# Performance work log

Hardware: AMD Instinct MI355X
Metric: run time of the kernel (lower is better)

Reference implementation:

```python
import jax, jax.numpy as jnp
import numpy as np

N, E, G = 50000, 500000, 64
IN_F, H_F, HEADS, OUT_F = 128, 64, 4, 326000
NEG_SLOPE = 0.2


def _gat_layer(h, W, a_src, a_dst, b, src, dst):
    # h: [N, H_F]; W: [H_F, HEADS*H_F]; a_src/a_dst: [HEADS, H_F]; b: [H_F]
    x = (h @ W).reshape(N, HEADS, H_F)                      # per-head transform
    ls = jnp.einsum('nhc,hc->nh', x, a_src)                  # [N, HEADS]
    ld = jnp.einsum('nhc,hc->nh', x, a_dst)
    e = jax.nn.leaky_relu(ls[src] + ld[dst], NEG_SLOPE)      # [E', HEADS] edge logits
    m = jax.ops.segment_max(e, dst, num_segments=N)          # segment-softmax (stable)
    m = jnp.where(jnp.isfinite(m), m, 0.0)
    ex = jnp.exp(e - m[dst])
    denom = jax.ops.segment_sum(ex, dst, num_segments=N)
    alpha = ex / (denom[dst] + 1e-16)                        # [E', HEADS]
    out = jax.ops.segment_sum(x[src] * alpha[:, :, None], dst, num_segments=N)  # [N,HEADS,H_F]
    return out.mean(axis=1) + b                              # concat=False -> head mean + bias


def setup_inputs() -> dict:
    key = jax.random.key(0)
    ks = jax.random.split(key, 24)
    inp = {
        'x': jax.random.normal(ks[0], (N, IN_F), dtype=jnp.float32),
        'edge_index': jax.random.randint(ks[1], (2, E), 0, N, dtype=jnp.int32),
        'edge_attr': jax.random.normal(ks[2], (E, 16), dtype=jnp.float32),
        'batch': jnp.sort(jax.random.randint(ks[3], (N,), 0, G, dtype=jnp.int32)),
        'W_emb': jax.random.normal(ks[4], (IN_F, H_F), dtype=jnp.float32) * 0.05,
        'b_emb': jnp.zeros((H_F,), dtype=jnp.float32),
        'W_fc': jax.random.normal(ks[5], (H_F, OUT_F), dtype=jnp.float32) * 0.05,
        'b_fc': jnp.zeros((OUT_F,), dtype=jnp.float32),
    }
    for l in range(3):
        inp[f'W{l+1}'] = jax.random.normal(ks[6 + 4 * l], (H_F, HEADS * H_F), dtype=jnp.float32) * 0.05
        inp[f'a_src{l+1}'] = jax.random.normal(ks[7 + 4 * l], (HEADS, H_F), dtype=jnp.float32) * 0.1
        inp[f'a_dst{l+1}'] = jax.random.normal(ks[8 + 4 * l], (HEADS, H_F), dtype=jnp.float32) * 0.1
        inp[f'b{l+1}'] = jnp.zeros((H_F,), dtype=jnp.float32)
    return inp


def reference(x, edge_index, edge_attr, batch, W_emb, b_emb,
              W1, a_src1, a_dst1, b1, W2, a_src2, a_dst2, b2,
              W3, a_src3, a_dst3, b3, W_fc, b_fc):
    # add self loops (PyG GATConv default)
    loop = jnp.arange(N, dtype=edge_index.dtype)
    src = jnp.concatenate([edge_index[0], loop])
    dst = jnp.concatenate([edge_index[1], loop])

    h = x @ W_emb + b_emb
    for (W, a_s, a_d, b) in ((W1, a_src1, a_dst1, b1), (W2, a_src2, a_dst2, b2), (W3, a_src3, a_dst3, b3)):
        h = jax.nn.relu(_gat_layer(h, W, a_s, a_d, b, src, dst))

    # global mean pool over graphs
    sums = jax.ops.segment_sum(h, batch, num_segments=G)
    cnt = jax.ops.segment_sum(jnp.ones((N,), h.dtype), batch, num_segments=G)
    pooled = sums / jnp.maximum(cnt, 1.0)[:, None]
    # dropout is identity in eval mode
    return pooled @ W_fc + b_fc
```

## Files before the change

### kernel.cpp

```cpp
#include <hip/hip_runtime.h>

#define NN 50000
#define EE 500000
#define GG 64
#define IN_F 128
#define H_F 64
#define HEADS 4
#define OUT_F 326000
#define NEG 0.2f
#define SCAN_B 256
#define NBLK ((NN + SCAN_B - 1) / SCAN_B)

__global__ __launch_bounds__(256) void k_emb(const float* __restrict__ x,
                                             const float* __restrict__ Wemb,
                                             const float* __restrict__ bemb,
                                             float* __restrict__ h0) {
    __shared__ float wlds[IN_F * H_F];
    int t = threadIdx.x;
#pragma unroll
    for (int i = 0; i < (IN_F * H_F) / (4 * 256); ++i)
        ((float4*)wlds)[t + 256 * i] = ((const float4*)Wemb)[t + 256 * i];
    __syncthreads();

    int c = t & 63, sub = t >> 6;
    int n0 = __builtin_amdgcn_readfirstlane(blockIdx.x * 32 + sub * 8);
    float bv = bemb[c];

    if (n0 + 8 <= NN) {
        const float4* xr = (const float4*)(x + (size_t)n0 * IN_F);
        float acc[8] = {0.f, 0.f, 0.f, 0.f, 0.f, 0.f, 0.f, 0.f};
        for (int k4 = 0; k4 < IN_F / 4; ++k4) {
            float w0 = wlds[(4 * k4 + 0) * H_F + c];
            float w1 = wlds[(4 * k4 + 1) * H_F + c];
            float w2 = wlds[(4 * k4 + 2) * H_F + c];
            float w3 = wlds[(4 * k4 + 3) * H_F + c];
#pragma unroll
            for (int j = 0; j < 8; ++j) {
                float4 xv = xr[j * (IN_F / 4) + k4];
                acc[j] = fmaf(xv.x, w0,
                         fmaf(xv.y, w1,
                         fmaf(xv.z, w2,
                         fmaf(xv.w, w3, acc[j]))));
            }
        }
#pragma unroll
        for (int j = 0; j < 8; ++j)
            h0[(size_t)(n0 + j) * H_F + c] = acc[j] + bv;
    } else {
        for (int j = 0; j < 8; ++j) {
            int n = n0 + j;
            if (n >= NN) break;
            const float* xrow = x + (size_t)n * IN_F;
            float a = 0.f;
            for (int k = 0; k < IN_F; ++k) a += xrow[k] * wlds[k * H_F + c];
            h0[(size_t)n * H_F + c] = a + bv;
        }
    }
}

__global__ void k_gemm_layer(const float* __restrict__ h, const float* __restrict__ W,
                             const float* __restrict__ a_src, const float* __restrict__ a_dst,
                             float* __restrict__ xbuf, float* __restrict__ ls,
                             float* __restrict__ ld) {
    int t = threadIdx.x;
    int lane = t & 63, wv = t >> 6;
    float wreg[H_F];
#pragma unroll
    for (int k = 0; k < H_F; ++k) wreg[k] = W[k * (HEADS * H_F) + t];
    float asv = a_src[t], adv = a_dst[t];
    int base = blockIdx.x * 32;
    for (int i = 0; i < 32; ++i) {
        int n = base + i;
        if (n >= NN) return;
        const float* hr = h + (size_t)n * H_F;
        float acc = 0.f;
#pragma unroll
        for (int k = 0; k < H_F; ++k) acc += hr[k] * wreg[k];
        xbuf[(size_t)n * (HEADS * H_F) + t] = acc;
        float vs = acc * asv, vd = acc * adv;
#pragma unroll
        for (int off = 32; off; off >>= 1) {
            vs += __shfl_xor(vs, off, 64);
            vd += __shfl_xor(vd, off, 64);
        }
        if (lane == 0) {
            ls[n * HEADS + wv] = vs;
            ld[n * HEADS + wv] = vd;
        }
    }
}

__device__ __forceinline__ float lrelu_exp(float e) {
    e = (e > 0.f) ? e : NEG * e;
    return __expf(e);
}

__global__ void k_count(const int* __restrict__ dst, int* __restrict__ cnt) {
    int i = blockIdx.x * blockDim.x + threadIdx.x;
    if (i >= EE + NN) return;
    int d = (i < EE) ? dst[i] : (i - EE);
    atomicAdd(&cnt[d], 1);
}

__global__ void k_scan1(const int* __restrict__ cnt, int* __restrict__ excl,
                        int* __restrict__ bsum) {
    __shared__ int lds[SCAN_B];
    int t = threadIdx.x, i = blockIdx.x * SCAN_B + t;
    int v = (i < NN) ? cnt[i] : 0;
    lds[t] = v;
    __syncthreads();
    for (int off = 1; off < SCAN_B; off <<= 1) {
        int add = (t >= off) ? lds[t - off] : 0;
        __syncthreads();
        lds[t] += add;
        __syncthreads();
    }
    if (i < NN) excl[i] = lds[t] - v;
    if (t == SCAN_B - 1) bsum[blockIdx.x] = lds[t];
}

__global__ void k_scan2(int* __restrict__ bsum) {
    __shared__ int lds[SCAN_B];
    int t = threadIdx.x;
    int v = (t < NBLK) ? bsum[t] : 0;
    lds[t] = v;
    __syncthreads();
    for (int off = 1; off < SCAN_B; off <<= 1) {
        int add = (t >= off) ? lds[t - off] : 0;
        __syncthreads();
        lds[t] += add;
        __syncthreads();
    }
    if (t < NBLK) bsum[t] = lds[t] - v;
}

__global__ void k_scan3(const int* __restrict__ excl, const int* __restrict__ bsum,
                        int* __restrict__ row, int* __restrict__ cursor) {
    int i = blockIdx.x * blockDim.x + threadIdx.x;
    if (i >= NN) return;
    int r = excl[i] + bsum[i / SCAN_B];
    row[i] = r;
    cursor[i] = r;
    if (i == 0) row[NN] = EE + NN;
}

__global__ void k_scatter(const int* __restrict__ src, const int* __restrict__ dst,
                          int* __restrict__ cursor, int* __restrict__ csr_src) {
    int i = blockIdx.x * blockDim.x + threadIdx.x;
    if (i >= EE + NN) return;
    int s, d;
    if (i < EE) { s = src[i]; d = dst[i]; } else { s = d = i - EE; }
    int pos = atomicAdd(&cursor[d], 1);
    csr_src[pos] = s;
}

__global__ __launch_bounds__(256) void k_aggr_csr(const int* __restrict__ row,
                                                  const int* __restrict__ csr_src,
                                                  const float4* __restrict__ ls4,
                                                  const float4* __restrict__ ld4,
                                                  const float* __restrict__ xbuf,
                                                  const float* __restrict__ bias,
                                                  float* __restrict__ hout) {
    int t = threadIdx.x;
    int lane = t & 63, wv = t >> 6;
    int d = blockIdx.x * 4 + wv;
    if (d >= NN) return;
    int r0 = row[d], r1 = row[d + 1];
    float4 bld = ld4[d];
    float den0 = 1e-16f, den1 = 1e-16f, den2 = 1e-16f, den3 = 1e-16f;
    float a0 = 0.f, a1 = 0.f, a2 = 0.f, a3 = 0.f;
    for (int j = r0; j < r1; ++j) {
        int s = __builtin_amdgcn_readfirstlane(csr_src[j]);
        float4 als = ls4[s];
        float e0 = lrelu_exp(als.x + bld.x);
        float e1 = lrelu_exp(als.y + bld.y);
        float e2 = lrelu_exp(als.z + bld.z);
        float e3 = lrelu_exp(als.w + bld.w);
        den0 += e0; den1 += e1; den2 += e2; den3 += e3;
        const float* xp = xbuf + (size_t)s * (HEADS * H_F);
        a0 = fmaf(e0, xp[lane], a0);
        a1 = fmaf(e1, xp[64 + lane], a1);
        a2 = fmaf(e2, xp[128 + lane], a2);
        a3 = fmaf(e3, xp[192 + lane], a3);
    }
    float res = 0.25f * (a0 / den0 + a1 / den1 + a2 / den2 + a3 / den3);
    res = fmaxf(res + bias[lane], 0.f);
    hout[(size_t)d * H_F + lane] = res;
}

__global__ void k_starts(const int* __restrict__ batch, int* __restrict__ starts) {
    int g = threadIdx.x;
    if (g > GG) return;
    int lo = 0, hi = NN;
    while (lo < hi) {
        int mid = (lo + hi) >> 1;
        if (batch[mid] < g) lo = mid + 1; else hi = mid;
    }
    starts[g] = lo;
}

__global__ void k_pool(const float* __restrict__ h, const int* __restrict__ starts,
                       float* __restrict__ pooledT) {
    int g = blockIdx.x;
    int s = starts[g], e = starts[g + 1];
    int t = threadIdx.x;
    int c = t & 63, j = t >> 6;
    float sum = 0.f;
    for (int n = s + j; n < e; n += 4) sum += h[(size_t)n * H_F + c];
    __shared__ float lds[256];
    lds[t] = sum;
    __syncthreads();
    if (j == 0) {
        float tot = lds[c] + lds[64 + c] + lds[128 + c] + lds[192 + c];
        int cnt = e - s;
        float inv = 1.0f / (float)(cnt > 0 ? cnt : 1);
        pooledT[c * GG + g] = tot * inv;
    }
}

__global__ __launch_bounds__(256) void k_fc(const float* __restrict__ pooledT,
                                            const float* __restrict__ Wfc,
                                            const float* __restrict__ bfc,
                                            float* __restrict__ out) {
    int o = blockIdx.x * blockDim.x + threadIdx.x;
    if (o >= OUT_F) return;
    float acc[GG];
#pragma unroll
    for (int g = 0; g < GG; ++g) acc[g] = 0.f;
    for (int c = 0; c < H_F; ++c) {
        float wvv = Wfc[(size_t)c * OUT_F + o];
        const float* pr = pooledT + c * GG;
#pragma unroll
        for (int g = 0; g < GG; ++g) acc[g] += pr[g] * wvv;
    }
    float bv = bfc[o];
    for (int g = 0; g < GG; ++g) out[(size_t)g * OUT_F + o] = acc[g] + bv;
}

extern "C" void kernel_launch(void* const* d_in, const int* in_sizes, int n_in,
                              void* d_out, int out_size, void* d_ws, size_t ws_size,
                              hipStream_t stream) {
    const float* x      = (const float*)d_in[0];
    const int*   eidx   = (const int*)d_in[1];
    const int*   batch  = (const int*)d_in[3];
    const float* W_emb  = (const float*)d_in[4];
    const float* b_emb  = (const float*)d_in[5];
    const float* W_fc   = (const float*)d_in[6];
    const float* b_fc   = (const float*)d_in[7];
    const float* Wl[3]   = {(const float*)d_in[8],  (const float*)d_in[12], (const float*)d_in[16]};
    const float* asl[3]  = {(const float*)d_in[9],  (const float*)d_in[13], (const float*)d_in[17]};
    const float* adl[3]  = {(const float*)d_in[10], (const float*)d_in[14], (const float*)d_in[18]};
    const float* bl[3]   = {(const float*)d_in[11], (const float*)d_in[15], (const float*)d_in[19]};

    const int* src = eidx;
    const int* dst = eidx + EE;

    float* xbuf    = (float*)d_ws;
    float* hA      = xbuf + (size_t)NN * 256;
    float* hB      = hA + (size_t)NN * 64;
    float* ls      = hB + (size_t)NN * 64;
    float* ldb     = ls + (size_t)NN * 4;
    float* pooledT = ldb + (size_t)NN * 4;
    int*   starts  = (int*)(pooledT + GG * GG);
    int*   cnt     = starts + 128;
    int*   excl    = cnt + NN;
    int*   bsum    = excl + NN;
    int*   row     = bsum + 256;
    int*   cursor  = row + NN + 4;
    int*   csr_src = cursor + NN;

    hipMemsetAsync(cnt, 0, (size_t)NN * sizeof(int), stream);
    k_count<<<(EE + NN + 255) / 256, 256, 0, stream>>>(dst, cnt);
    k_scan1<<<NBLK, SCAN_B, 0, stream>>>(cnt, excl, bsum);
    k_scan2<<<1, SCAN_B, 0, stream>>>(bsum);
    k_scan3<<<(NN + 255) / 256, 256, 0, stream>>>(excl, bsum, row, cursor);
    k_scatter<<<(EE + NN + 255) / 256, 256, 0, stream>>>(src, dst, cursor, csr_src);

    k_emb<<<(NN + 31) / 32, 256, 0, stream>>>(x, W_emb, b_emb, hA);

    float* hcur = hA;
    float* hnext = hB;
    for (int l = 0; l < 3; ++l) {
        k_gemm_layer<<<(NN + 31) / 32, 256, 0, stream>>>(hcur, Wl[l], asl[l], adl[l],
                                                         xbuf, ls, ldb);
        k_aggr_csr<<<(NN + 3) / 4, 256, 0, stream>>>(row, csr_src,
                                                     (const float4*)ls, (const float4*)ldb,
                                                     xbuf, bl[l], hnext);
        float* tmp = hcur; hcur = hnext; hnext = tmp;
    }

    k_starts<<<1, 128, 0, stream>>>(batch, starts);
    k_pool<<<GG, 256, 0, stream>>>(hcur, starts, pooledT);
    k_fc<<<(OUT_F + 255) / 256, 256, 0, stream>>>(pooledT, W_fc, b_fc, (float*)d_out);
}
```

Before: 821.1 us.

## Interleave head features in xbuf and process two destinations per wave in aggregation

The GEMM kernel now writes transformed features interleaved by head (lane*4+head), so the aggregation kernel can fetch all four heads' values for a lane as a single float4 load. Each wave now handles two destination nodes at once, interleaving their edge loops and prefetching the next source index, to expose more memory-level parallelism in the gather. The GEMM also computes two nodes per iteration with split accumulators to reuse the weight registers. The grid becomes NN/8, which relies on NN being divisible by 8, and uneven degree pairs fall back to tail loops.

```diff
diff --git a/kernel.cpp b/kernel.cpp
--- a/kernel.cpp
+++ b/kernel.cpp
@@ -69,23 +69,37 @@
     for (int k = 0; k < H_F; ++k) wreg[k] = W[k * (HEADS * H_F) + t];
     float asv = a_src[t], adv = a_dst[t];
     int base = blockIdx.x * 32;
-    for (int i = 0; i < 32; ++i) {
-        int n = base + i;
-        if (n >= NN) return;
-        const float* hr = h + (size_t)n * H_F;
-        float acc = 0.f;
-#pragma unroll
-        for (int k = 0; k < H_F; ++k) acc += hr[k] * wreg[k];
-        xbuf[(size_t)n * (HEADS * H_F) + t] = acc;
-        float vs = acc * asv, vd = acc * adv;
-#pragma unroll
-        for (int off = 32; off; off >>= 1) {
-            vs += __shfl_xor(vs, off, 64);
-            vd += __shfl_xor(vd, off, 64);
+    for (int i = 0; i < 32; i += 2) {
+        int n0 = base + i;
+        if (n0 >= NN) return;
+        int n1 = n0 + 1;
+        const float* h0r = h + (size_t)n0 * H_F;
+        const float* h1r = h + (size_t)n1 * H_F;
+        float a0 = 0.f, a1 = 0.f, b0 = 0.f, b1 = 0.f;
+#pragma unroll
+        for (int k = 0; k < H_F; k += 2) {
+            a0 = fmaf(h0r[k], wreg[k], a0);
+            a1 = fmaf(h0r[k + 1], wreg[k + 1], a1);
+            b0 = fmaf(h1r[k], wreg[k], b0);
+            b1 = fmaf(h1r[k + 1], wreg[k + 1], b1);
         }
-        if (lane == 0) {
-            ls[n * HEADS + wv] = vs;
-            ld[n * HEADS + wv] = vd;
+        float acc0 = a0 + a1, acc1 = b0 + b1;
+        xbuf[(size_t)n0 * (HEADS * H_F) + lane * 4 + wv] = acc0;
+        xbuf[(size_t)n1 * (HEADS * H_F) + lane * 4 + wv] = acc1;
+#pragma unroll
+        for (int rep = 0; rep < 2; ++rep) {
+            float acc = rep ? acc1 : acc0;
+            int n = rep ? n1 : n0;
+            float vs = acc * asv, vd = acc * adv;
+#pragma unroll
+            for (int off = 32; off; off >>= 1) {
+                vs += __shfl_xor(vs, off, 64);
+                vd += __shfl_xor(vd, off, 64);
+            }
+            if (lane == 0) {
+                ls[n * HEADS + wv] = vs;
+                ld[n * HEADS + wv] = vd;
+            }
         }
     }
 }
@@ -93,6 +107,15 @@
 __device__ __forceinline__ float lrelu_exp(float e) {
     e = (e > 0.f) ? e : NEG * e;
     return __expf(e);
+}
+
+__device__ __forceinline__ float4 lexp4(float4 s, float4 d) {
+    float4 r;
+    r.x = lrelu_exp(s.x + d.x);
+    r.y = lrelu_exp(s.y + d.y);
+    r.z = lrelu_exp(s.z + d.z);
+    r.w = lrelu_exp(s.w + d.w);
+    return r;
 }
 
 __global__ void k_count(const int* __restrict__ dst, int* __restrict__ cnt) {
@@ -158,34 +181,79 @@
                                                   const int* __restrict__ csr_src,
                                                   const float4* __restrict__ ls4,
                                                   const float4* __restrict__ ld4,
-                                                  const float* __restrict__ xbuf,
+                                                  const float4* __restrict__ xb4,
                                                   const float* __restrict__ bias,
                                                   float* __restrict__ hout) {
     int t = threadIdx.x;
     int lane = t & 63, wv = t >> 6;
-    int d = blockIdx.x * 4 + wv;
-    if (d >= NN) return;
-    int r0 = row[d], r1 = row[d + 1];
-    float4 bld = ld4[d];
-    float den0 = 1e-16f, den1 = 1e-16f, den2 = 1e-16f, den3 = 1e-16f;
-    float a0 = 0.f, a1 = 0.f, a2 = 0.f, a3 = 0.f;
-    for (int j = r0; j < r1; ++j) {
-        int s = __builtin_amdgcn_readfirstlane(csr_src[j]);
-        float4 als = ls4[s];
-        float e0 = lrelu_exp(als.x + bld.x);
-        float e1 = lrelu_exp(als.y + bld.y);
-        float e2 = lrelu_exp(als.z + bld.z);
-        float e3 = lrelu_exp(als.w + bld.w);
-        den0 += e0; den1 += e1; den2 += e2; den3 += e3;
-        const float* xp = xbuf + (size_t)s * (HEADS * H_F);
-        a0 = fmaf(e0, xp[lane], a0);
-        a1 = fmaf(e1, xp[64 + lane], a1);
-        a2 = fmaf(e2, xp[128 + lane], a2);
-        a3 = fmaf(e3, xp[192 + lane], a3);
-    }
-    float res = 0.25f * (a0 / den0 + a1 / den1 + a2 / den2 + a3 / den3);
-    res = fmaxf(res + bias[lane], 0.f);
-    hout[(size_t)d * H_F + lane] = res;
+    int dA = blockIdx.x * 8 + wv * 2;
+    int dB = dA + 1;
+    if (dA >= NN) return;
+    int r0A = row[dA], r1A = row[dA + 1];
+    int r0B = row[dB], r1B = row[dB + 1];
+    float4 bldA = ld4[dA];
+    float4 bldB = ld4[dB];
+    float4 accA = {0.f, 0.f, 0.f, 0.f}, denA = {1e-16f, 1e-16f, 1e-16f, 1e-16f};
+    float4 accB = {0.f, 0.f, 0.f, 0.f}, denB = {1e-16f, 1e-16f, 1e-16f, 1e-16f};
+
+    int jA = r0A, jB = r0B;
+    int sA = (jA < r1A) ? csr_src[jA] : 0;
+    int sB = (jB < r1B) ? csr_src[jB] : 0;
+
+    while (jA < r1A && jB < r1B) {
+        int sa = __builtin_amdgcn_readfirstlane(sA);
+        int sb = __builtin_amdgcn_readfirstlane(sB);
+        float4 xa = xb4[(size_t)sa * H_F + lane];
+        float4 xb = xb4[(size_t)sb * H_F + lane];
+        float4 la = ls4[sa];
+        float4 lb = ls4[sb];
+        ++jA; if (jA < r1A) sA = csr_src[jA];
+        ++jB; if (jB < r1B) sB = csr_src[jB];
+        float4 ea = lexp4(la, bldA);
+        float4 eb = lexp4(lb, bldB);
+        denA.x += ea.x; denA.y += ea.y; denA.z += ea.z; denA.w += ea.w;
+        denB.x += eb.x; denB.y += eb.y; denB.z += eb.z; denB.w += eb.w;
+        accA.x = fmaf(ea.x, xa.x, accA.x);
+        accA.y = fmaf(ea.y, xa.y, accA.y);
+        accA.z = fmaf(ea.z, xa.z, accA.z);
+        accA.w = fmaf(ea.w, xa.w, accA.w);
+        accB.x = fmaf(eb.x, xb.x, accB.x);
+        accB.y = fmaf(eb.y, xb.y, accB.y);
+        accB.z = fmaf(eb.z, xb.z, accB.z);
+        accB.w = fmaf(eb.w, xb.w, accB.w);
+    }
+    while (jA < r1A) {
+        int sa = __builtin_amdgcn_readfirstlane(sA);
+        float4 xa = xb4[(size_t)sa * H_F + lane];
+        float4 la = ls4[sa];
+        ++jA; if (jA < r1A) sA = csr_src[jA];
+        float4 ea = lexp4(la, bldA);
+        denA.x += ea.x; denA.y += ea.y; denA.z += ea.z; denA.w += ea.w;
+        accA.x = fmaf(ea.x, xa.x, accA.x);
+        accA.y = fmaf(ea.y, xa.y, accA.y);
+        accA.z = fmaf(ea.z, xa.z, accA.z);
+        accA.w = fmaf(ea.w, xa.w, accA.w);
+    }
+    while (jB < r1B) {
+        int sb = __builtin_amdgcn_readfirstlane(sB);
+        float4 xb = xb4[(size_t)sb * H_F + lane];
+        float4 lb = ls4[sb];
+        ++jB; if (jB < r1B) sB = csr_src[jB];
+        float4 eb = lexp4(lb, bldB);
+        denB.x += eb.x; denB.y += eb.y; denB.z += eb.z; denB.w += eb.w;
+        accB.x = fmaf(eb.x, xb.x, accB.x);
+        accB.y = fmaf(eb.y, xb.y, accB.y);
+        accB.z = fmaf(eb.z, xb.z, accB.z);
+        accB.w = fmaf(eb.w, xb.w, accB.w);
+    }
+
+    float bv = bias[lane];
+    float resA = 0.25f * (accA.x / denA.x + accA.y / denA.y +
+                          accA.z / denA.z + accA.w / denA.w);
+    float resB = 0.25f * (accB.x / denB.x + accB.y / denB.y +
+                          accB.z / denB.z + accB.w / denB.w);
+    hout[(size_t)dA * H_F + lane] = fmaxf(resA + bv, 0.f);
+    hout[(size_t)dB * H_F + lane] = fmaxf(resB + bv, 0.f);
 }
 
 __global__ void k_starts(const int* __restrict__ batch, int* __restrict__ starts) {
@@ -283,9 +351,9 @@
     for (int l = 0; l < 3; ++l) {
         k_gemm_layer<<<(NN + 31) / 32, 256, 0, stream>>>(hcur, Wl[l], asl[l], adl[l],
                                                          xbuf, ls, ldb);
-        k_aggr_csr<<<(NN + 3) / 4, 256, 0, stream>>>(row, csr_src,
-                                                     (const float4*)ls, (const float4*)ldb,
-                                                     xbuf, bl[l], hnext);
+        k_aggr_csr<<<NN / 8, 256, 0, stream>>>(row, csr_src,
+                                               (const float4*)ls, (const float4*)ldb,
+                                               (const float4*)xbuf, bl[l], hnext);
         float* tmp = hcur; hcur = hnext; hnext = tmp;
     }
 
```

Result: slower. 1.021 ms (+24.4%).
